# Kernel optimization log

Measured on AMD Instinct MI355X. Metric: run time of the kernel, lower is better.

The kernel has to match this reference:

```python
import jax, jax.numpy as jnp
import numpy as np
from jax import lax

B, L, DIN, DOUT, K = 8, 4096, 256, 256, 3


def _gates(x, W, b, k):
    # x: [B, L, Din] -> conv over time, channels-first like torch Conv1d
    xt = jnp.transpose(x, (0, 2, 1))  # [B, Din, L]
    pad = (k - 1) // 2
    g = lax.conv_general_dilated(xt, W, window_strides=(1,), padding=[(pad, pad)],
                                 dimension_numbers=("NCH", "OIH", "NCH"))
    g = g + b[None, :, None]
    g = jnp.transpose(g, (0, 2, 1))  # [B, L, 3*Dout]
    f, o, z = jnp.split(g, 3, axis=-1)
    return jax.nn.sigmoid(f), jax.nn.sigmoid(o), jnp.tanh(z)


def _fo_pool(f, z, init_cell, reverse):
    # c_t = f_t * c_{t-1} + (1 - f_t) * z_t ; scan over time axis
    fT = jnp.transpose(f, (1, 0, 2))  # [L, B, D]
    zT = jnp.transpose(z, (1, 0, 2))

    def step(c, fz):
        ft, zt = fz
        c = ft * c + (1.0 - ft) * zt
        return c, c

    _, cells = lax.scan(step, init_cell, (fT, zT), reverse=reverse)
    return jnp.transpose(cells, (1, 0, 2))  # [B, L, D]


def setup_inputs() -> dict:
    key = jax.random.key(0)
    k1, k2, k3, k4, k5, k6 = jax.random.split(key, 6)
    scale_in = 1.0 / np.sqrt(DIN * K)
    inp = {
        "input": jax.random.normal(k1, (B, L, DIN), dtype=jnp.float32),
        "lengths": jnp.full((B,), L, dtype=jnp.int64) if False else jax.random.randint(k2, (B,), 1, L + 1),
        "W_fwd": jax.random.uniform(k3, (3 * DOUT, DIN, K), dtype=jnp.float32, minval=-scale_in, maxval=scale_in),
        "b_fwd": jax.random.uniform(k4, (3 * DOUT,), dtype=jnp.float32, minval=-scale_in, maxval=scale_in),
        "W_bwd": jax.random.uniform(k5, (3 * DOUT, DIN, K), dtype=jnp.float32, minval=-scale_in, maxval=scale_in),
        "b_bwd": jax.random.uniform(k6, (3 * DOUT,), dtype=jnp.float32, minval=-scale_in, maxval=scale_in),
    }
    return inp


def reference(input, lengths, W_fwd, b_fwd, W_bwd, b_bwd):
    init_cell = jnp.zeros((input.shape[0], DOUT), dtype=input.dtype)

    # forward direction
    f, o, z = _gates(input, W_fwd, b_fwd, K)
    cell = _fo_pool(f, z, init_cell, reverse=False)
    hidden = cell * o

    # backward direction
    fr, orr, zr = _gates(input, W_bwd, b_bwd, K)
    rcell = _fo_pool(fr, zr, init_cell, reverse=True)
    rhidden = rcell * orr

    output = jnp.concatenate([hidden, rhidden], axis=-1)  # [B, L, 2*Dout]
    last_h = jnp.concatenate([hidden[:, -1, :], rhidden[:, -1, :]], axis=-1)
    last_c = jnp.concatenate([cell[:, -1, :], rcell[:, -1, :]], axis=-1)
    return output, last_h, last_c
```

## Files before the change

### kernel.cpp

```cpp
#include <hip/hip_runtime.h>
#include <hip/hip_bf16.h>
#include <hip/hip_fp16.h>

#define B_     8
#define L_     4096
#define DIN    256
#define DOUT   256
#define NGATE  1536
#define KDIM   768
#define LP     (L_ + 2)
#define CHUNK  32
#define NCHUNK (L_ / CHUNK)

typedef short    short8  __attribute__((ext_vector_type(8)));
typedef __bf16   bf16x8  __attribute__((ext_vector_type(8)));
typedef float    floatx4 __attribute__((ext_vector_type(4)));
typedef _Float16 half4   __attribute__((ext_vector_type(4)));

__device__ __forceinline__ float fast_sigmoid(float x) {
    return __builtin_amdgcn_rcpf(1.f + __expf(-x));
}
__device__ __forceinline__ float fast_tanh(float x) {
    return 1.f - 2.f * __builtin_amdgcn_rcpf(1.f + __expf(2.f * x));
}
__device__ __forceinline__ unsigned short f2bf(float x) {
    unsigned u = __float_as_uint(x);
    u += 0x7FFF + ((u >> 16) & 1);
    return (unsigned short)(u >> 16);
}
__device__ __forceinline__ void gload16(const unsigned short* g, unsigned short* l) {
    __builtin_amdgcn_global_load_lds((const __attribute__((address_space(1))) void*)g,
                                     (__attribute__((address_space(3))) void*)l,
                                     16, 0, 0);
}

__device__ __forceinline__ int gate_noff(int n) {
    return (n >> 7) * 32768 + ((n >> 6) & 1) * 4096 + ((n >> 4) & 3) * 1024 + (n & 15) * 4;
}
__device__ __forceinline__ int gate_toff(int b, int t) {
    return (b * 16 + (t >> 8)) * 393216 + ((t >> 6) & 3) * 8192
         + ((t >> 4) & 3) * 256 + ((t >> 2) & 3) * 64;
}

#define NXB ((B_ * LP * 64 + 255) / 256)
#define NWB ((NGATE * KDIM + 255) / 256)
__global__ void prep_all(const float* __restrict__ x, unsigned short* __restrict__ Xp,
                         const float* __restrict__ Wf, const float* __restrict__ bf_,
                         const float* __restrict__ Wb, const float* __restrict__ bb,
                         unsigned short* __restrict__ Wc, float* __restrict__ bc) {
    if (blockIdx.x < NXB) {
        int idx = blockIdx.x * 256 + threadIdx.x;
        int row = idx >> 6;
        if (row >= B_ * LP) return;
        int c4 = (idx & 63) << 2;
        int b = row / LP, r = row - b * LP;
        float4 v = make_float4(0.f, 0.f, 0.f, 0.f);
        if (r >= 1 && r <= L_) {
            v = *(const float4*)(x + ((size_t)(b * L_ + (r - 1))) * DIN + c4);
        }
        ushort4 o = make_ushort4(f2bf(v.x), f2bf(v.y), f2bf(v.z), f2bf(v.w));
        *(ushort4*)(Xp + (size_t)row * DIN + c4) = o;
    } else {
        int gid = (blockIdx.x - NXB) * 256 + threadIdx.x;
        if (gid < NGATE) {
            bc[gid] = (gid < 768) ? bf_[gid] : bb[gid - 768];
        }
        if (gid >= NGATE * KDIM) return;
        int n = gid / KDIM, k = gid - n * KDIM;
        int s = k >> 8, ic = k & 255;
        const float* W = (n < 768) ? Wf : Wb;
        int oc = (n < 768) ? n : n - 768;
        float v = W[(size_t)oc * KDIM + ic * 3 + s];
        Wc[(size_t)n * KDIM + k] = f2bf(v);
    }
}

__launch_bounds__(512)
__global__ void gemm_gates(const unsigned short* __restrict__ Xp,
                           const unsigned short* __restrict__ Wc,
                           const float* __restrict__ bc,
                           _Float16* __restrict__ gates) {
    __shared__ unsigned short As[256 * 64];
    __shared__ unsigned short Bs[128 * 64];
    const int tid  = threadIdx.x;
    const int lane = tid & 63, wave = tid >> 6;
    const int quad = lane >> 4, l16 = lane & 15;
    const int wr = wave >> 1, wcl = wave & 1;

    int flat = blockIdx.x;
    int xcd  = flat & 7;
    int slot = flat >> 3;
    int bm   = xcd * 16 + slot / 12;
    int nblk = slot % 12;
    const int b  = bm >> 4;
    const int t0 = (bm & 15) << 8;
    const int n0 = nblk << 7;
    const unsigned short* Ab = Xp + (size_t)b * LP * DIN;

    int rowA[4], cgA[4], rowB[2], cgB[2];
#pragma unroll
    for (int j = 0; j < 4; j++) {
        int G = (wave * 4 + j) * 64 + lane;
        rowA[j] = G >> 3;
        cgA[j]  = ((G & 7) ^ (rowA[j] & 7)) * 8;
    }
#pragma unroll
    for (int j = 0; j < 2; j++) {
        int G = (wave * 2 + j) * 64 + lane;
        rowB[j] = G >> 3;
        cgB[j]  = ((G & 7) ^ (rowB[j] & 7)) * 8;
    }

    floatx4 acc[4][4];
#pragma unroll
    for (int i = 0; i < 4; i++)
#pragma unroll
        for (int j = 0; j < 4; j++) acc[i][j] = (floatx4)0.f;

    for (int k0 = 0; k0 < KDIM; k0 += 64) {
        const int sh = k0 >> 8;
        const int c0 = k0 & 255;
#pragma unroll
        for (int j = 0; j < 4; j++)
            gload16(Ab + (size_t)(t0 + rowA[j] + sh) * DIN + c0 + cgA[j],
                    &As[(wave * 4 + j) * 512]);
#pragma unroll
        for (int j = 0; j < 2; j++)
            gload16(Wc + (size_t)(n0 + rowB[j]) * KDIM + k0 + cgB[j],
                    &Bs[(wave * 2 + j) * 512]);
        __syncthreads();
#pragma unroll
        for (int kk = 0; kk < 2; kk++) {
            const int g0 = kk * 4 + quad;
            short8 af[4], bfr[4];
#pragma unroll
            for (int mi = 0; mi < 4; mi++) {
                int row = wr * 64 + mi * 16 + l16;
                af[mi] = *(const short8*)&As[row * 64 + ((g0 ^ (row & 7)) << 3)];
            }
#pragma unroll
            for (int ni = 0; ni < 4; ni++) {
                int row = wcl * 64 + ni * 16 + l16;
                bfr[ni] = *(const short8*)&Bs[row * 64 + ((g0 ^ (row & 7)) << 3)];
            }
#pragma unroll
            for (int mi = 0; mi < 4; mi++)
#pragma unroll
                for (int ni = 0; ni < 4; ni++)
                    acc[mi][ni] = __builtin_amdgcn_mfma_f32_16x16x32_bf16(
                        __builtin_bit_cast(bf16x8, af[mi]),
                        __builtin_bit_cast(bf16x8, bfr[ni]),
                        acc[mi][ni], 0, 0, 0);
        }
        __syncthreads();
    }

    const int cls = ((n0 + wcl * 64) >> 8) % 3;
    _Float16* gb = gates + ((size_t)(bm * 12 + nblk) * 8 + wave) * 4096 + lane * 4;
#pragma unroll
    for (int ni = 0; ni < 4; ni++) {
        float bias = bc[n0 + wcl * 64 + ni * 16 + l16];
#pragma unroll
        for (int mi = 0; mi < 4; mi++) {
            half4 hv;
#pragma unroll
            for (int rr = 0; rr < 4; rr++) {
                float v = acc[mi][ni][rr] + bias;
                v = (cls == 2) ? fast_tanh(v) : fast_sigmoid(v);
                hv[rr] = (_Float16)v;
            }
            *(half4*)(gb + (ni * 4 + mi) * 256) = hv;
        }
    }
}

__global__ void scan_chunks(const _Float16* __restrict__ gates,
                            float2* __restrict__ PW) {
    const int d = threadIdx.x;
    const int s = blockIdx.x, b = blockIdx.y, dir = blockIdx.z;
    const int onf = gate_noff(dir * 768 + d);
    const int onz = gate_noff(dir * 768 + 512 + d);
    float P = 1.f, W = 0.f;
    if (dir == 0) {
#pragma unroll
        for (int gi = 0; gi < 8; gi++) {
            int t = s * CHUNK + gi * 4;
            int ot = gate_toff(b, t);
            half4 f4 = *(const half4*)(gates + ot + onf);
            half4 z4 = *(const half4*)(gates + ot + onz);
#pragma unroll
            for (int u = 0; u < 4; u++) {
                float f = (float)f4[u], z = (float)z4[u];
                W = f * W + (1.f - f) * z;
                P *= f;
            }
        }
    } else {
#pragma unroll
        for (int gi = 7; gi >= 0; gi--) {
            int t = s * CHUNK + gi * 4;
            int ot = gate_toff(b, t);
            half4 f4 = *(const half4*)(gates + ot + onf);
            half4 z4 = *(const half4*)(gates + ot + onz);
#pragma unroll
            for (int u = 3; u >= 0; u--) {
                float f = (float)f4[u], z = (float)z4[u];
                W = f * W + (1.f - f) * z;
                P *= f;
            }
        }
    }
    PW[(((size_t)(dir * 8 + b)) * NCHUNK + s) * 256 + d] = make_float2(P, W);
}

__global__ void scan_seq(const float2* __restrict__ PW, float* __restrict__ C0) {
    const int c = threadIdx.x;
    const int dir = blockIdx.x >> 3, b = blockIdx.x & 7;
    const size_t base = ((size_t)(dir * 8 + b)) * NCHUNK * 256 + c;
    float cc = 0.f;
    if (dir == 0) {
#pragma unroll 16
        for (int s = 0; s < NCHUNK; s++) {
            float2 pw = PW[base + (size_t)s * 256];
            C0[base + (size_t)s * 256] = cc;
            cc = pw.x * cc + pw.y;
        }
    } else {
#pragma unroll 16
        for (int s = NCHUNK - 1; s >= 0; s--) {
            float2 pw = PW[base + (size_t)s * 256];
            C0[base + (size_t)s * 256] = cc;
            cc = pw.x * cc + pw.y;
        }
    }
}

__global__ void scan_final(const _Float16* __restrict__ gates,
                           const float* __restrict__ C0,
                           float* __restrict__ out) {
    __shared__ float hbuf[4][256];
    const int d = threadIdx.x;
    const int s = blockIdx.x, b = blockIdx.y, dir = blockIdx.z;
    const int onf = gate_noff(dir * 768 + d);
    const int ono = gate_noff(dir * 768 + 256 + d);
    const int onz = gate_noff(dir * 768 + 512 + d);
    float c = C0[(((size_t)(dir * 8 + b)) * NCHUNK + s) * 256 + d];
    float* ob = out + (size_t)(b * L_) * (2 * DOUT) + dir * DOUT;
    float* lasth = out + (size_t)B_ * L_ * (2 * DOUT);
    float* lastc = lasth + B_ * (2 * DOUT);
    const int tl = d >> 6, cl = (d & 63) * 4;

    for (int gg = 0; gg < 8; gg++) {
        int gi = (dir == 0) ? gg : 7 - gg;
        int t = s * CHUNK + gi * 4;
        int ot = gate_toff(b, t);
        half4 f4 = *(const half4*)(gates + ot + onf);
        half4 o4 = *(const half4*)(gates + ot + ono);
        half4 z4 = *(const half4*)(gates + ot + onz);
        float h[4];
        if (dir == 0) {
#pragma unroll
            for (int u = 0; u < 4; u++) {
                float f = (float)f4[u], z = (float)z4[u];
                c = f * c + (1.f - f) * z;
                h[u] = c * (float)o4[u];
            }
            if (s == NCHUNK - 1 && gi == 7) {
                lasth[b * 2 * DOUT + d] = h[3];
                lastc[b * 2 * DOUT + d] = c;
            }
        } else {
#pragma unroll
            for (int u = 3; u >= 0; u--) {
                float f = (float)f4[u], z = (float)z4[u];
                c = f * c + (1.f - f) * z;
                h[u] = c * (float)o4[u];
                if (u == 3 && s == NCHUNK - 1 && gi == 7) {
                    lasth[b * 2 * DOUT + DOUT + d] = h[3];
                    lastc[b * 2 * DOUT + DOUT + d] = c;
                }
            }
        }
        hbuf[0][d] = h[0];
        hbuf[1][d] = h[1];
        hbuf[2][d] = h[2];
        hbuf[3][d] = h[3];
        __syncthreads();
        *(float4*)&ob[(size_t)(t + tl) * (2 * DOUT) + cl] = *(float4*)&hbuf[tl][cl];
        __syncthreads();
    }
}

extern "C" void kernel_launch(void* const* d_in, const int* in_sizes, int n_in,
                              void* d_out, int out_size, void* d_ws, size_t ws_size,
                              hipStream_t stream) {
    const float* x   = (const float*)d_in[0];
    const float* Wf  = (const float*)d_in[2];
    const float* bfv = (const float*)d_in[3];
    const float* Wb  = (const float*)d_in[4];
    const float* bbv = (const float*)d_in[5];

    char* ws = (char*)d_ws;
    unsigned short* Xp    = (unsigned short*)(ws);
    unsigned short* Wc    = (unsigned short*)(ws + 16785408);
    float*          bc    = (float*)(ws + 19144704);
    _Float16*       gates = (_Float16*)(ws + 19150848);
    float2*         PW    = (float2*)(ws);
    float*          C0    = (float*)(ws + 4194304);
    float*          out   = (float*)d_out;

    prep_all<<<NXB + NWB, 256, 0, stream>>>(x, Xp, Wf, bfv, Wb, bbv, Wc, bc);
    gemm_gates<<<1536, 512, 0, stream>>>(Xp, Wc, bc, gates);
    scan_chunks<<<dim3(NCHUNK, B_, 2), 256, 0, stream>>>(gates, PW);
    scan_seq<<<16, 256, 0, stream>>>(PW, C0);
    scan_final<<<dim3(NCHUNK, B_, 2), 256, 0, stream>>>(gates, C0, out);
}
```

Measured before the change: 215.8 us.

## Switch gate GEMM to 32x32 MFMA and batch scan output stores per chunk

```diff
diff --git a/kernel.cpp b/kernel.cpp
--- a/kernel.cpp
+++ b/kernel.cpp
@@ -12,10 +12,10 @@
 #define CHUNK  32
 #define NCHUNK (L_ / CHUNK)
 
-typedef short    short8  __attribute__((ext_vector_type(8)));
-typedef __bf16   bf16x8  __attribute__((ext_vector_type(8)));
-typedef float    floatx4 __attribute__((ext_vector_type(4)));
-typedef _Float16 half4   __attribute__((ext_vector_type(4)));
+typedef short    short8   __attribute__((ext_vector_type(8)));
+typedef __bf16   bf16x8   __attribute__((ext_vector_type(8)));
+typedef float    floatx16 __attribute__((ext_vector_type(16)));
+typedef _Float16 half4    __attribute__((ext_vector_type(4)));
 
 __device__ __forceinline__ float fast_sigmoid(float x) {
     return __builtin_amdgcn_rcpf(1.f + __expf(-x));
@@ -35,11 +35,11 @@
 }
 
 __device__ __forceinline__ int gate_noff(int n) {
-    return (n >> 7) * 32768 + ((n >> 6) & 1) * 4096 + ((n >> 4) & 3) * 1024 + (n & 15) * 4;
+    return (n >> 7) * 32768 + ((n >> 6) & 1) * 4096 + ((n >> 5) & 1) * 2048 + (n & 31) * 4;
 }
 __device__ __forceinline__ int gate_toff(int b, int t) {
     return (b * 16 + (t >> 8)) * 393216 + ((t >> 6) & 3) * 8192
-         + ((t >> 4) & 3) * 256 + ((t >> 2) & 3) * 64;
+         + ((t >> 5) & 1) * 1024 + ((t >> 3) & 3) * 256 + ((t >> 2) & 1) * 128 + (t & 3);
 }
 
 #define NXB ((B_ * LP * 64 + 255) / 256)
@@ -84,7 +84,7 @@
     __shared__ unsigned short Bs[128 * 64];
     const int tid  = threadIdx.x;
     const int lane = tid & 63, wave = tid >> 6;
-    const int quad = lane >> 4, l16 = lane & 15;
+    const int l31 = lane & 31, lhi = lane >> 5;
     const int wr = wave >> 1, wcl = wave & 1;
 
     int flat = blockIdx.x;
@@ -111,11 +111,11 @@
         cgB[j]  = ((G & 7) ^ (rowB[j] & 7)) * 8;
     }
 
-    floatx4 acc[4][4];
-#pragma unroll
-    for (int i = 0; i < 4; i++)
-#pragma unroll
-        for (int j = 0; j < 4; j++) acc[i][j] = (floatx4)0.f;
+    floatx16 acc[2][2];
+#pragma unroll
+    for (int i = 0; i < 2; i++)
+#pragma unroll
+        for (int j = 0; j < 2; j++) acc[i][j] = (floatx16)0.f;
 
     for (int k0 = 0; k0 < KDIM; k0 += 64) {
         const int sh = k0 >> 8;
@@ -130,46 +130,49 @@
                     &Bs[(wave * 2 + j) * 512]);
         __syncthreads();
 #pragma unroll
-        for (int kk = 0; kk < 2; kk++) {
-            const int g0 = kk * 4 + quad;
-            short8 af[4], bfr[4];
-#pragma unroll
-            for (int mi = 0; mi < 4; mi++) {
-                int row = wr * 64 + mi * 16 + l16;
-                af[mi] = *(const short8*)&As[row * 64 + ((g0 ^ (row & 7)) << 3)];
-            }
-#pragma unroll
-            for (int ni = 0; ni < 4; ni++) {
-                int row = wcl * 64 + ni * 16 + l16;
-                bfr[ni] = *(const short8*)&Bs[row * 64 + ((g0 ^ (row & 7)) << 3)];
-            }
-#pragma unroll
-            for (int mi = 0; mi < 4; mi++)
-#pragma unroll
-                for (int ni = 0; ni < 4; ni++)
-                    acc[mi][ni] = __builtin_amdgcn_mfma_f32_16x16x32_bf16(
-                        __builtin_bit_cast(bf16x8, af[mi]),
-                        __builtin_bit_cast(bf16x8, bfr[ni]),
-                        acc[mi][ni], 0, 0, 0);
+        for (int ks = 0; ks < 4; ks++) {
+            const int gsel = ks * 2 + lhi;
+            short8 af[2], bfr[2];
+#pragma unroll
+            for (int ms = 0; ms < 2; ms++) {
+                int row = wr * 64 + ms * 32 + l31;
+                af[ms] = *(const short8*)&As[row * 64 + ((gsel ^ (row & 7)) << 3)];
+            }
+#pragma unroll
+            for (int ns = 0; ns < 2; ns++) {
+                int row = wcl * 64 + ns * 32 + l31;
+                bfr[ns] = *(const short8*)&Bs[row * 64 + ((gsel ^ (row & 7)) << 3)];
+            }
+#pragma unroll
+            for (int ms = 0; ms < 2; ms++)
+#pragma unroll
+                for (int ns = 0; ns < 2; ns++)
+                    acc[ms][ns] = __builtin_amdgcn_mfma_f32_32x32x16_bf16(
+                        __builtin_bit_cast(bf16x8, af[ms]),
+                        __builtin_bit_cast(bf16x8, bfr[ns]),
+                        acc[ms][ns], 0, 0, 0);
         }
         __syncthreads();
     }
 
-    const int cls = ((n0 + wcl * 64) >> 8) % 3;
+    const int cls = (nblk >> 1) % 3;
     _Float16* gb = gates + ((size_t)(bm * 12 + nblk) * 8 + wave) * 4096 + lane * 4;
 #pragma unroll
-    for (int ni = 0; ni < 4; ni++) {
-        float bias = bc[n0 + wcl * 64 + ni * 16 + l16];
-#pragma unroll
-        for (int mi = 0; mi < 4; mi++) {
-            half4 hv;
-#pragma unroll
-            for (int rr = 0; rr < 4; rr++) {
-                float v = acc[mi][ni][rr] + bias;
-                v = (cls == 2) ? fast_tanh(v) : fast_sigmoid(v);
-                hv[rr] = (_Float16)v;
-            }
-            *(half4*)(gb + (ni * 4 + mi) * 256) = hv;
+    for (int ns = 0; ns < 2; ns++) {
+        float bias = bc[n0 + wcl * 64 + ns * 32 + l31];
+#pragma unroll
+        for (int ms = 0; ms < 2; ms++) {
+#pragma unroll
+            for (int g = 0; g < 4; g++) {
+                half4 hv;
+#pragma unroll
+                for (int rr = 0; rr < 4; rr++) {
+                    float v = acc[ms][ns][g * 4 + rr] + bias;
+                    v = (cls == 2) ? fast_tanh(v) : fast_sigmoid(v);
+                    hv[rr] = (_Float16)v;
+                }
+                *(half4*)(gb + ns * 2048 + ms * 1024 + g * 256) = hv;
+            }
         }
     }
 }
@@ -238,56 +241,69 @@
 __global__ void scan_final(const _Float16* __restrict__ gates,
                            const float* __restrict__ C0,
                            float* __restrict__ out) {
-    __shared__ float hbuf[4][256];
+    __shared__ float hbuf[CHUNK][256];
     const int d = threadIdx.x;
     const int s = blockIdx.x, b = blockIdx.y, dir = blockIdx.z;
     const int onf = gate_noff(dir * 768 + d);
     const int ono = gate_noff(dir * 768 + 256 + d);
     const int onz = gate_noff(dir * 768 + 512 + d);
     float c = C0[(((size_t)(dir * 8 + b)) * NCHUNK + s) * 256 + d];
-    float* ob = out + (size_t)(b * L_) * (2 * DOUT) + dir * DOUT;
-    float* lasth = out + (size_t)B_ * L_ * (2 * DOUT);
-    float* lastc = lasth + B_ * (2 * DOUT);
-    const int tl = d >> 6, cl = (d & 63) * 4;
-
-    for (int gg = 0; gg < 8; gg++) {
-        int gi = (dir == 0) ? gg : 7 - gg;
-        int t = s * CHUNK + gi * 4;
-        int ot = gate_toff(b, t);
-        half4 f4 = *(const half4*)(gates + ot + onf);
-        half4 o4 = *(const half4*)(gates + ot + ono);
-        half4 z4 = *(const half4*)(gates + ot + onz);
-        float h[4];
-        if (dir == 0) {
+    float lh = 0.f, lc = 0.f;
+
+    if (dir == 0) {
+#pragma unroll
+        for (int gi = 0; gi < 8; gi++) {
+            int t = s * CHUNK + gi * 4;
+            int ot = gate_toff(b, t);
+            half4 f4 = *(const half4*)(gates + ot + onf);
+            half4 o4 = *(const half4*)(gates + ot + ono);
+            half4 z4 = *(const half4*)(gates + ot + onz);
 #pragma unroll
             for (int u = 0; u < 4; u++) {
                 float f = (float)f4[u], z = (float)z4[u];
                 c = f * c + (1.f - f) * z;
-                h[u] = c * (float)o4[u];
-            }
-            if (s == NCHUNK - 1 && gi == 7) {
-                lasth[b * 2 * DOUT + d] = h[3];
-                lastc[b * 2 * DOUT + d] = c;
-            }
-        } else {
+                float h = c * (float)o4[u];
+                hbuf[gi * 4 + u][d] = h;
+                lh = h;
+            }
+        }
+        lc = c;
+    } else {
+#pragma unroll
+        for (int gg = 0; gg < 8; gg++) {
+            int gi = 7 - gg;
+            int t = s * CHUNK + gi * 4;
+            int ot = gate_toff(b, t);
+            half4 f4 = *(const half4*)(gates + ot + onf);
+            half4 o4 = *(const half4*)(gates + ot + ono);
+            half4 z4 = *(const half4*)(gates + ot + onz);
 #pragma unroll
             for (int u = 3; u >= 0; u--) {
                 float f = (float)f4[u], z = (float)z4[u];
                 c = f * c + (1.f - f) * z;
-                h[u] = c * (float)o4[u];
-                if (u == 3 && s == NCHUNK - 1 && gi == 7) {
-                    lasth[b * 2 * DOUT + DOUT + d] = h[3];
-                    lastc[b * 2 * DOUT + DOUT + d] = c;
-                }
-            }
-        }
-        hbuf[0][d] = h[0];
-        hbuf[1][d] = h[1];
-        hbuf[2][d] = h[2];
-        hbuf[3][d] = h[3];
-        __syncthreads();
-        *(float4*)&ob[(size_t)(t + tl) * (2 * DOUT) + cl] = *(float4*)&hbuf[tl][cl];
-        __syncthreads();
+                float h = c * (float)o4[u];
+                hbuf[gi * 4 + u][d] = h;
+                if (gg == 0 && u == 3) { lh = h; lc = c; }
+            }
+        }
+    }
+    if (s == NCHUNK - 1) {
+        float* lasth = out + (size_t)B_ * L_ * (2 * DOUT);
+        float* lastc = lasth + B_ * (2 * DOUT);
+        lasth[b * 2 * DOUT + dir * DOUT + d] = lh;
+        lastc[b * 2 * DOUT + dir * DOUT + d] = lc;
+    }
+    __syncthreads();
+
+    const float* hb = &hbuf[0][0];
+    const size_t obase = ((size_t)(b * L_) + s * CHUNK) * (2 * DOUT) + dir * DOUT;
+#pragma unroll
+    for (int i = 0; i < 8; i++) {
+        int chunk = i * 256 + d;
+        int row = chunk >> 6;
+        int col = (chunk & 63) * 4;
+        *(float4*)&out[obase + (size_t)row * (2 * DOUT) + col] =
+            *(const float4*)&hb[row * 256 + col];
     }
 }
 
```

After: 220.6 us. 1.02x slower.
